# Kernel tuning notes

Measured on AMD Instinct MI355X. Metric: run time of the kernel, lower is better.

## Reference

```python
import jax, jax.numpy as jnp
import numpy as np

TAU = 10.0
EPS = 1e-6
TOP_K = 8


def setup_inputs() -> dict:
    key = jax.random.key(0)
    ks = jax.random.split(key, 5)
    D, NB, H = 1024, 512, 4096
    B, S = 4, 2048
    x = jax.random.normal(ks[0], (B, S, D), dtype=jnp.float32)
    W1 = jax.random.normal(ks[1], (H, D), dtype=jnp.float32) * (1.0 / np.sqrt(D))
    W2 = jax.random.normal(ks[2], (D, H), dtype=jnp.float32) * (1.0 / np.sqrt(H))
    ln_g = jnp.ones((D,), jnp.float32)
    ln_b = jnp.zeros((D,), jnp.float32)
    router_W = jax.random.normal(ks[3], (NB, D), dtype=jnp.float32) * 0.01
    router_b = jnp.zeros((NB,), jnp.float32)
    raw_U = jax.random.normal(ks[4], (NB, D), dtype=jnp.float32) * 0.02
    raw_V = jax.random.normal(jax.random.fold_in(key, 7), (NB, D), dtype=jnp.float32) * 0.02
    gamma = jnp.ones((1, 1, D), jnp.float32) * 0.1
    return {"x": x, "W1": W1, "W2": W2, "ln_g": ln_g, "ln_b": ln_b,
            "router_W": router_W, "router_b": router_b,
            "raw_U": raw_U, "raw_V": raw_V, "gamma": gamma}


def _layernorm(x, g, b):
    mu = jnp.mean(x, axis=-1, keepdims=True)
    var = jnp.var(x, axis=-1, keepdims=True)
    return (x - mu) * jax.lax.rsqrt(var + 1e-5) * g + b


def _unit_rows(W):
    n = jnp.linalg.norm(W, axis=1, keepdims=True)
    return W / jnp.maximum(n, EPS)


def reference(x, W1, W2, ln_g, ln_b, router_W, router_b, raw_U, raw_V, gamma):
    B, S, D = x.shape
    x_flat = x.reshape(-1, D)                      # [N, D]
    r_raw = _layernorm(x_flat, ln_g, ln_b) @ router_W.T + router_b  # [N, NB]
    r = jnp.clip(r_raw, -TAU, TAU)
    alpha = jax.nn.softplus(r)
    phi, idx = jax.lax.top_k(alpha, TOP_K)         # [N, K]
    S_sum = jnp.sum(phi, axis=-1, keepdims=True)
    Z = (phi / (S_sum + EPS)) * jnp.tanh(S_sum)    # [N, K]
    U_sel = _unit_rows(raw_U)[idx]                 # [N, K, D]
    V_sel = _unit_rows(raw_V)[idx]                 # [N, K, D]
    h_lat = jnp.einsum('nd,nkd->nk', x_flat, U_sel)
    dyn = jnp.einsum('nk,nkd->nd', h_lat * Z, V_sel).reshape(B, S, D) * gamma
    static = (jax.nn.gelu(x_flat @ W1.T, approximate=False) @ W2.T).reshape(B, S, D)
    return static + dyn
```

## Files before the change

### kernel.cpp

```cpp
#include <hip/hip_runtime.h>
#include <hip/hip_bf16.h>
#include <math.h>

#define N_TOK 8192
#define DDIM  1024
#define HDIM  4096
#define NBLK  512

typedef __bf16 bf16x8 __attribute__((ext_vector_type(8)));
typedef __bf16 bf16x4 __attribute__((ext_vector_type(4)));
typedef float  floatx4 __attribute__((ext_vector_type(4)));

__device__ __forceinline__ float wave_reduce_sum(float v) {
#pragma unroll
    for (int off = 32; off > 0; off >>= 1) v += __shfl_down(v, off, 64);
    return v;
}

__device__ __forceinline__ void gload_lds16(const void* g, void* l) {
    __builtin_amdgcn_global_load_lds((const __attribute__((address_space(1))) void*)g,
                                     (__attribute__((address_space(3))) void*)l,
                                     16, 0, 0);
}

__device__ __forceinline__ float fast_gelu(float x) {
    float ax = fabsf(x);
    float z  = ax * 0.70710678118654752f;
    float t  = __builtin_amdgcn_rcpf(fmaf(0.3275911f, z, 1.0f));
    float p  = fmaf(fmaf(fmaf(fmaf(1.061405429f, t, -1.453152027f),
                              t, 1.421413741f),
                         t, -0.284496736f),
                    t, 0.254829592f);
    p *= t;
    float e = __expf(-z * z);
    float E = fmaf(-p, e, 1.0f);
    return 0.5f * fmaf(ax, E, x);
}

__device__ __forceinline__ float fast_softplus(float r) {
    return __logf(fmaf(1.0f, __expf(r), 1.0f));
}

__device__ __forceinline__ void cast1024(const float* __restrict__ s,
                                         __bf16* __restrict__ d,
                                         size_t off, int t) {
    float4 v = ((const float4*)(s + off))[t];
    bf16x4 o;
    o.x = (__bf16)v.x; o.y = (__bf16)v.y;
    o.z = (__bf16)v.z; o.w = (__bf16)v.w;
    ((bf16x4*)(d + off))[t] = o;
}

__global__ __launch_bounds__(256) void prep_kernel(
        const float* __restrict__ x,
        const float* __restrict__ ln_g, const float* __restrict__ ln_b,
        const float* __restrict__ W1,   const float* __restrict__ W2,
        const float* __restrict__ router_W,
        const float* __restrict__ rawU, const float* __restrict__ rawV,
        __bf16* __restrict__ xb,  __bf16* __restrict__ lnb,
        __bf16* __restrict__ w1b, __bf16* __restrict__ w2b,
        __bf16* __restrict__ rwb,
        float* __restrict__ unitU, float* __restrict__ unitV) {
    int b = blockIdx.x;
    int t = threadIdx.x;

    if (b < 1024) {
        const float* src = (b < NBLK) ? rawU + (size_t)b * DDIM
                                      : rawV + (size_t)(b - NBLK) * DDIM;
        float* dst = (b < NBLK) ? unitU + (size_t)b * DDIM
                                : unitV + (size_t)(b - NBLK) * DDIM;
        float vals[4];
        float ss = 0.f;
#pragma unroll
        for (int i = 0; i < 4; i++) { vals[i] = src[t + i * 256]; ss += vals[i] * vals[i]; }
        __shared__ float red[4];
        ss = wave_reduce_sum(ss);
        if ((t & 63) == 0) red[t >> 6] = ss;
        __syncthreads();
        float tot = red[0] + red[1] + red[2] + red[3];
        float inv = 1.f / fmaxf(sqrtf(tot), 1e-6f);
#pragma unroll
        for (int i = 0; i < 4; i++) dst[t + i * 256] = vals[i] * inv;
    } else if (b < 9216) {
        int n = b - 1024;
        const float* row = x + (size_t)n * DDIM;
        float v[4];
        float s1 = 0.f, s2 = 0.f;
#pragma unroll
        for (int i = 0; i < 4; i++) {
            v[i] = row[t + i * 256];
            s1 += v[i];
            s2 += v[i] * v[i];
        }
        __shared__ float r1[4], r2[4];
        s1 = wave_reduce_sum(s1);
        s2 = wave_reduce_sum(s2);
        if ((t & 63) == 0) { r1[t >> 6] = s1; r2[t >> 6] = s2; }
        __syncthreads();
        float mu  = (r1[0] + r1[1] + r1[2] + r1[3]) * (1.f / DDIM);
        float var = (r2[0] + r2[1] + r2[2] + r2[3]) * (1.f / DDIM) - mu * mu;
        float rstd = rsqrtf(var + 1e-5f);
        __bf16* orow = lnb + (size_t)n * DDIM;
        __bf16* xrow = xb  + (size_t)n * DDIM;
#pragma unroll
        for (int i = 0; i < 4; i++) {
            int d = t + i * 256;
            orow[d] = (__bf16)((v[i] - mu) * rstd * ln_g[d] + ln_b[d]);
            xrow[d] = (__bf16)v[i];
        }
    } else if (b < 13312) {
        cast1024(W1, w1b, (size_t)(b - 9216) * 1024, t);
    } else if (b < 17408) {
        cast1024(W2, w2b, (size_t)(b - 13312) * 1024, t);
    } else {
        cast1024(router_W, rwb, (size_t)(b - 17408) * 1024, t);
    }
}

template <int MODE, int BN>
__global__ __launch_bounds__(256) void mfma_gemm(const __bf16* __restrict__ A,
                                                 const __bf16* __restrict__ B,
                                                 const float* __restrict__ bias,
                                                 void* __restrict__ Cv,
                                                 int M, int Nn, int Kk) {
    constexpr int NJ  = BN / 32;
    constexpr int NQB = BN / 64;
    __shared__ __align__(16) __bf16 As[2][128 * 32];
    __shared__ __align__(16) __bf16 Bs[2][BN * 32];

    const int t    = threadIdx.x;
    const int lane = t & 63;
    const int wave = t >> 6;
    const int wm   = wave >> 1, wn = wave & 1;
    const int lr   = lane & 15, quad = lane >> 4;
    const int m0   = blockIdx.x * 128;
    const int n0   = blockIdx.y * BN;

    const int ca0 = t & 3;
    const __bf16* Ag[2];
    const __bf16* Bg[NQB];
    int ldsOffA[2], ldsOffB[NQB];
#pragma unroll
    for (int q = 0; q < 2; q++) {
        int idx = q * 256 + t;
        Ag[q]      = A + (size_t)(m0 + (idx >> 2)) * Kk + ca0 * 8;
        ldsOffA[q] = idx * 8;
    }
#pragma unroll
    for (int q = 0; q < NQB; q++) {
        int idx = q * 256 + t;
        Bg[q]      = B + (size_t)(n0 + (idx >> 2)) * Kk + ca0 * 8;
        ldsOffB[q] = idx * 8;
    }

    int raOff[4], rbOff[NJ];
#pragma unroll
    for (int i = 0; i < 4; i++)
        raOff[i] = (wm * 64 + i * 16 + lr) * 32 + quad * 8;
#pragma unroll
    for (int j = 0; j < NJ; j++)
        rbOff[j] = (wn * (BN / 2) + j * 16 + lr) * 32 + quad * 8;

    floatx4 acc[4][NJ];
#pragma unroll
    for (int i = 0; i < 4; i++)
#pragma unroll
        for (int j = 0; j < NJ; j++) acc[i][j] = (floatx4)0.f;

#pragma unroll
    for (int q = 0; q < 2; q++)   gload_lds16(Ag[q], &As[0][ldsOffA[q]]);
#pragma unroll
    for (int q = 0; q < NQB; q++) gload_lds16(Bg[q], &Bs[0][ldsOffB[q]]);

    const int niter = Kk >> 5;
    for (int it = 0; it < niter; ++it) {
        const int cur = it & 1;
        __syncthreads();
        if (it + 1 < niter) {
            const int nk = (it + 1) << 5;
            const int nb = cur ^ 1;
#pragma unroll
            for (int q = 0; q < 2; q++)   gload_lds16(Ag[q] + nk, &As[nb][ldsOffA[q]]);
#pragma unroll
            for (int q = 0; q < NQB; q++) gload_lds16(Bg[q] + nk, &Bs[nb][ldsOffB[q]]);
        }
        bf16x8 af[4], bfr[NJ];
#pragma unroll
        for (int i = 0; i < 4; i++)  af[i]  = *(const bf16x8*)&As[cur][raOff[i]];
#pragma unroll
        for (int j = 0; j < NJ; j++) bfr[j] = *(const bf16x8*)&Bs[cur][rbOff[j]];
#pragma unroll
        for (int i = 0; i < 4; i++)
#pragma unroll
            for (int j = 0; j < NJ; j++)
                acc[i][j] = __builtin_amdgcn_mfma_f32_16x16x32_bf16(af[i], bfr[j],
                                                                    acc[i][j], 0, 0, 0);
    }

    const int mBase = m0 + wm * 64 + quad * 4;
    const int nBase = n0 + wn * (BN / 2) + lr;
#pragma unroll
    for (int i = 0; i < 4; i++) {
#pragma unroll
        for (int j = 0; j < NJ; j++) {
            int n = nBase + j * 16;
#pragma unroll
            for (int r = 0; r < 4; r++) {
                int m = mBase + i * 16 + r;
                float v = acc[i][j][r];
                if (MODE == 0) {
                    float rr = v + bias[n];
                    rr = fminf(fmaxf(rr, -10.f), 10.f);
                    ((float*)Cv)[(size_t)m * Nn + n] = fast_softplus(rr);
                } else if (MODE == 1) {
                    ((__bf16*)Cv)[(size_t)m * Nn + n] = (__bf16)fast_gelu(v);
                } else {
                    ((float*)Cv)[(size_t)m * Nn + n] += v;
                }
            }
        }
    }
}

template <int MODE, int SPLITK>
__global__ __launch_bounds__(512, 2) void mfma_gemm8v2(const __bf16* __restrict__ A,
                                                       const __bf16* __restrict__ B,
                                                       void* __restrict__ Cv,
                                                       int M, int Nn, int Kk) {
    __shared__ __align__(16) __bf16 As[2][256 * 64];
    __shared__ __align__(16) __bf16 Bs[2][256 * 64];

    const int t    = threadIdx.x;
    const int lane = t & 63;
    const int wave = t >> 6;
    const int wm   = wave >> 2;
    const int wn   = wave & 3;
    const int lr   = lane & 15, quad = lane >> 4;

    const int nbn   = Nn >> 8;
    const int nmb   = M >> 8;
    const int chunk = gridDim.x >> 3;
    const int bid   = blockIdx.x;
    const int wg    = (bid & 7) * chunk + (bid >> 3);
    const int kslc  = wg / (nmb * nbn);
    const int rem   = wg % (nmb * nbn);
    const int m0    = (rem / nbn) * 256;
    const int n0    = (rem % nbn) * 256;
    const int kseg  = Kk / SPLITK;
    const int NT    = kseg >> 6;

    const int srow = t >> 3;
    const int scb  = ((t & 7) << 4) ^ ((srow & 7) << 4);
    const __bf16* aP = A + (size_t)(m0 + srow) * Kk + (size_t)kslc * kseg + (scb >> 1);
    const __bf16* bP = B + (size_t)(n0 + srow) * Kk + (size_t)kslc * kseg + (scb >> 1);
    const int dP = srow * 64 + (t & 7) * 8;

    int aRd[2], bRd[2];
#pragma unroll
    for (int ks = 0; ks < 2; ks++) {
        int sw = ((ks * 64 + quad * 16) ^ ((lr & 7) << 4)) >> 1;
        aRd[ks] = (wm * 64 + lr) * 64 + sw;
        bRd[ks] = (wn * 32 + lr) * 64 + sw;
    }

    floatx4 acc[8][4];
#pragma unroll
    for (int i = 0; i < 8; i++)
#pragma unroll
        for (int j = 0; j < 4; j++) acc[i][j] = (floatx4)0.f;

    bf16x8 af[4][2];
    bf16x8 bfr0[2][2];
    bf16x8 bfr1[2][2];

#define STAGE_A(KT, MH, BUF)                                                        \
    _Pragma("unroll") for (int q = 0; q < 2; q++)                                   \
        gload_lds16(aP + (size_t)(KT) * 64 + (size_t)(q * 64 + (MH) * 128) * Kk,    \
                    &As[BUF][dP + (q * 64 + (MH) * 128) * 64])
#define STAGE_B(KT, NH, BUF)                                                        \
    _Pragma("unroll") for (int q = 0; q < 2; q++)                                   \
        gload_lds16(bP + (size_t)(KT) * 64 + (size_t)(q * 64 + (NH) * 128) * Kk,    \
                    &Bs[BUF][dP + (q * 64 + (NH) * 128) * 64])
#define LDA(CUR, MH)                                                                \
    _Pragma("unroll") for (int ii = 0; ii < 4; ii++)                                \
    _Pragma("unroll") for (int ks = 0; ks < 2; ks++)                                \
        af[ii][ks] = *(const bf16x8*)&As[CUR][aRd[ks] + (MH) * 8192 + ii * 1024]
#define LDB(CUR, NH, DST)                                                           \
    _Pragma("unroll") for (int jj = 0; jj < 2; jj++)                                \
    _Pragma("unroll") for (int ks = 0; ks < 2; ks++)                                \
        DST[jj][ks] = *(const bf16x8*)&Bs[CUR][bRd[ks] + ((NH) * 128 + jj * 16) * 64]
#define MM(MH, NH, BFR)                                                             \
    _Pragma("unroll") for (int ii = 0; ii < 4; ii++)                                \
    _Pragma("unroll") for (int jj = 0; jj < 2; jj++)                                \
    _Pragma("unroll") for (int ks = 0; ks < 2; ks++)                                \
        acc[(MH) * 4 + ii][(NH) * 2 + jj] =                                         \
            __builtin_amdgcn_mfma_f32_16x16x32_bf16(                                \
                af[ii][ks], BFR[jj][ks], acc[(MH) * 4 + ii][(NH) * 2 + jj], 0, 0, 0)
#define VWAIT(NSTR) asm volatile("s_waitcnt vmcnt(" NSTR ")" ::: "memory")
#define LHINT()     asm volatile("s_waitcnt lgkmcnt(8)" ::: "memory")
#define WAITL()     asm volatile("s_waitcnt lgkmcnt(0)" ::: "memory")
#define BARR()      __builtin_amdgcn_s_barrier()
#define PRIO1()     __builtin_amdgcn_s_setprio(1)
#define PRIO0()     __builtin_amdgcn_s_setprio(0)

#define TILE(KT, CUR, ST1, ST2, VM)                                                 \
    do {                                                                            \
        LDA(CUR, 0); LDB(CUR, 0, bfr0);                                             \
        if (ST1) { STAGE_A((KT) + 1, 1, ((KT) + 1) & 1); }                          \
        LHINT(); BARR(); WAITL();                                                   \
        PRIO1(); MM(0, 0, bfr0); PRIO0(); BARR();                                   \
        LDB(CUR, 1, bfr1);                                                          \
        if (ST2) { STAGE_A((KT) + 2, 0, (KT) & 1); }                                \
        BARR(); WAITL();                                                            \
        PRIO1(); MM(0, 1, bfr1); PRIO0(); BARR();                                   \
        LDA(CUR, 1);                                                                \
        if (ST2) { STAGE_B((KT) + 2, 0, (KT) & 1); }                                \
        BARR(); WAITL();                                                            \
        PRIO1(); MM(1, 1, bfr1); PRIO0(); BARR();                                   \
        if (ST2) { STAGE_B((KT) + 2, 1, (KT) & 1); }                                \
        VWAIT(VM); BARR();                                                          \
        PRIO1(); MM(1, 0, bfr0); PRIO0(); BARR();                                   \
    } while (0)

    STAGE_A(0, 0, 0); STAGE_B(0, 0, 0); STAGE_B(0, 1, 0); STAGE_A(0, 1, 0);
    STAGE_A(1, 0, 1); STAGE_B(1, 0, 1); STAGE_B(1, 1, 1);
    VWAIT("6");
    BARR();

    for (int kt = 0; kt < NT - 2; ++kt)
        TILE(kt, kt & 1, true, true, "6");
    TILE(NT - 2, (NT - 2) & 1, true, false, "0");
    TILE(NT - 1, (NT - 1) & 1, false, false, "0");

#undef STAGE_A
#undef STAGE_B
#undef LDA
#undef LDB
#undef MM
#undef VWAIT
#undef LHINT
#undef WAITL
#undef BARR
#undef PRIO1
#undef PRIO0
#undef TILE

#pragma unroll
    for (int i = 0; i < 8; i++) {
        const int mh = i >> 2, ii = i & 3;
#pragma unroll
        for (int j = 0; j < 4; j++) {
            const int nh = j >> 1, jj = j & 1;
            const int n = n0 + nh * 128 + wn * 32 + jj * 16 + lr;
#pragma unroll
            for (int r = 0; r < 4; r++) {
                const int m = m0 + mh * 128 + wm * 64 + ii * 16 + quad * 4 + r;
                const float v = acc[i][j][r];
                if (MODE == 1) {
                    ((__bf16*)Cv)[(size_t)m * Nn + n] = (__bf16)fast_gelu(v);
                } else {
                    atomicAdd(&((float*)Cv)[(size_t)m * Nn + n], v);
                }
            }
        }
    }
}

__global__ __launch_bounds__(256) void topk_dyn_kernel(
        const float* __restrict__ alpha,
        const float* __restrict__ x,
        const float* __restrict__ unitU,
        const float* __restrict__ unitV,
        const float* __restrict__ gamma,
        float* __restrict__ out) {
    int n = blockIdx.x;
    int t = threadIdx.x;
    int lane = t & 63, wid = t >> 6;

    __shared__ int   sidx[8];
    __shared__ float shz[8];
    __shared__ float red[8][4];
    __shared__ float hz[8];

    if (wid == 0) {
        const float* row = alpha + (size_t)n * NBLK;
        float v[8];
#pragma unroll
        for (int i = 0; i < 8; i++) v[i] = row[lane + i * 64];
        float topv[8];
        int   topi[8];
        for (int s = 0; s < 8; s++) {
            float bv = v[0]; int bi = 0;
#pragma unroll
            for (int i = 1; i < 8; i++)
                if (v[i] > bv) { bv = v[i]; bi = i; }
            int gidx = lane + bi * 64;
#pragma unroll
            for (int off = 1; off < 64; off <<= 1) {
                float ov = __shfl_xor(bv, off, 64);
                int   oi = __shfl_xor(gidx, off, 64);
                if (ov > bv || (ov == bv && oi < gidx)) { bv = ov; gidx = oi; }
            }
            topv[s] = bv; topi[s] = gidx;
            if ((gidx & 63) == lane) v[gidx >> 6] = -1e30f;
        }
        float S = 0.f;
#pragma unroll
        for (int s = 0; s < 8; s++) S += topv[s];
        float zscale = tanhf(S) / (S + 1e-6f);
        if (lane < 8) {
            sidx[lane] = topi[lane];
            shz[lane]  = topv[lane] * zscale;
        }
    }
    __syncthreads();

    const float* xr = x + (size_t)n * DDIM;
    float xv[4];
#pragma unroll
    for (int i = 0; i < 4; i++) xv[i] = xr[t + i * 256];

    float acc[8];
#pragma unroll
    for (int k = 0; k < 8; k++) {
        const float* ur = unitU + (size_t)sidx[k] * DDIM;
        float a = 0.f;
#pragma unroll
        for (int i = 0; i < 4; i++) a = fmaf(xv[i], ur[t + i * 256], a);
        acc[k] = a;
    }
#pragma unroll
    for (int k = 0; k < 8; k++) {
        float a = wave_reduce_sum(acc[k]);
        if (lane == 0) red[k][wid] = a;
    }
    __syncthreads();
    if (t < 8) {
        float h = red[t][0] + red[t][1] + red[t][2] + red[t][3];
        hz[t] = h * shz[t];
    }
    __syncthreads();

    float* orow = out + (size_t)n * DDIM;
#pragma unroll
    for (int i = 0; i < 4; i++) {
        int d = t + i * 256;
        float s = 0.f;
#pragma unroll
        for (int k = 0; k < 8; k++)
            s = fmaf(hz[k], unitV[(size_t)sidx[k] * DDIM + d], s);
        orow[d] = s * gamma[d];
    }
}

extern "C" void kernel_launch(void* const* d_in, const int* in_sizes, int n_in,
                              void* d_out, int out_size, void* d_ws, size_t ws_size,
                              hipStream_t stream) {
    const float* x        = (const float*)d_in[0];
    const float* W1       = (const float*)d_in[1];
    const float* W2       = (const float*)d_in[2];
    const float* ln_g     = (const float*)d_in[3];
    const float* ln_b     = (const float*)d_in[4];
    const float* router_W = (const float*)d_in[5];
    const float* router_b = (const float*)d_in[6];
    const float* raw_U    = (const float*)d_in[7];
    const float* raw_V    = (const float*)d_in[8];
    const float* gamma    = (const float*)d_in[9];
    float* out = (float*)d_out;

    char* ws = (char*)d_ws;
    __bf16* lnb   = (__bf16*)(ws);
    float*  alpha = (float*)(ws + 16777216u);
    __bf16* g1    = (__bf16*)(ws);
    __bf16* xb    = (__bf16*)(ws + 67108864u);
    __bf16* w1b   = (__bf16*)(ws + 83886080u);
    __bf16* w2b   = (__bf16*)(ws + 92274688u);
    __bf16* rwb   = (__bf16*)(ws + 100663296u);
    float*  unitU = (float*)(ws + 101711872u);
    float*  unitV = (float*)(ws + 103809024u);

    prep_kernel<<<17920, 256, 0, stream>>>(x, ln_g, ln_b, W1, W2, router_W,
                                           raw_U, raw_V, xb, lnb, w1b, w2b, rwb,
                                           unitU, unitV);

    dim3 gR(N_TOK / 128, NBLK / 64);
    mfma_gemm<0, 64><<<gR, 256, 0, stream>>>(lnb, rwb, router_b, (void*)alpha,
                                             N_TOK, NBLK, DDIM);

    topk_dyn_kernel<<<N_TOK, 256, 0, stream>>>(alpha, x, unitU, unitV, gamma, out);

    mfma_gemm8v2<1, 1><<<dim3(512), dim3(512), 0, stream>>>(xb, w1b, (void*)g1,
                                                            N_TOK, HDIM, DDIM);

    mfma_gemm8v2<2, 2><<<dim3(256), dim3(512), 0, stream>>>(g1, w2b, (void*)out,
                                                            N_TOK, DDIM, HDIM);
}
```

Before: 371.5 us.

## Add finer-grained vmcnt pipeline schedule for first GEMM and vectorize elementwise kernels

Adds a template schedule parameter to the 256x256 MFMA GEMM. The first GEMM (x·W1ᵀ with GELU) now uses a variant that waits on global-to-LDS loads at several points inside each K tile, keeping more loads in flight rather than waiting once per tile. The second GEMM keeps the old schedule. The prep and top-k/dynamic kernels are switched to float4/bf16x4 vector loads and stores to cut memory instruction count. The vmcnt thresholds are hand-tuned, so a wrong value could cause a read of LDS data that has not arrived yet.

Measured after the change: 369.2 us, median of 2. About the same (-0.6%).

```diff
diff --git a/kernel.cpp b/kernel.cpp
--- a/kernel.cpp
+++ b/kernel.cpp
@@ -69,29 +69,22 @@
                                       : rawV + (size_t)(b - NBLK) * DDIM;
         float* dst = (b < NBLK) ? unitU + (size_t)b * DDIM
                                 : unitV + (size_t)(b - NBLK) * DDIM;
-        float vals[4];
-        float ss = 0.f;
-#pragma unroll
-        for (int i = 0; i < 4; i++) { vals[i] = src[t + i * 256]; ss += vals[i] * vals[i]; }
+        float4 v = ((const float4*)src)[t];
+        float ss = v.x * v.x + v.y * v.y + v.z * v.z + v.w * v.w;
         __shared__ float red[4];
         ss = wave_reduce_sum(ss);
         if ((t & 63) == 0) red[t >> 6] = ss;
         __syncthreads();
         float tot = red[0] + red[1] + red[2] + red[3];
         float inv = 1.f / fmaxf(sqrtf(tot), 1e-6f);
-#pragma unroll
-        for (int i = 0; i < 4; i++) dst[t + i * 256] = vals[i] * inv;
+        float4 o;
+        o.x = v.x * inv; o.y = v.y * inv; o.z = v.z * inv; o.w = v.w * inv;
+        ((float4*)dst)[t] = o;
     } else if (b < 9216) {
         int n = b - 1024;
-        const float* row = x + (size_t)n * DDIM;
-        float v[4];
-        float s1 = 0.f, s2 = 0.f;
-#pragma unroll
-        for (int i = 0; i < 4; i++) {
-            v[i] = row[t + i * 256];
-            s1 += v[i];
-            s2 += v[i] * v[i];
-        }
+        float4 v = ((const float4*)(x + (size_t)n * DDIM))[t];
+        float s1 = v.x + v.y + v.z + v.w;
+        float s2 = v.x * v.x + v.y * v.y + v.z * v.z + v.w * v.w;
         __shared__ float r1[4], r2[4];
         s1 = wave_reduce_sum(s1);
         s2 = wave_reduce_sum(s2);
@@ -100,14 +93,17 @@
         float mu  = (r1[0] + r1[1] + r1[2] + r1[3]) * (1.f / DDIM);
         float var = (r2[0] + r2[1] + r2[2] + r2[3]) * (1.f / DDIM) - mu * mu;
         float rstd = rsqrtf(var + 1e-5f);
-        __bf16* orow = lnb + (size_t)n * DDIM;
-        __bf16* xrow = xb  + (size_t)n * DDIM;
-#pragma unroll
-        for (int i = 0; i < 4; i++) {
-            int d = t + i * 256;
-            orow[d] = (__bf16)((v[i] - mu) * rstd * ln_g[d] + ln_b[d]);
-            xrow[d] = (__bf16)v[i];
-        }
+        float4 g  = ((const float4*)ln_g)[t];
+        float4 bb = ((const float4*)ln_b)[t];
+        bf16x4 o, xo;
+        o.x = (__bf16)((v.x - mu) * rstd * g.x + bb.x);
+        o.y = (__bf16)((v.y - mu) * rstd * g.y + bb.y);
+        o.z = (__bf16)((v.z - mu) * rstd * g.z + bb.z);
+        o.w = (__bf16)((v.w - mu) * rstd * g.w + bb.w);
+        xo.x = (__bf16)v.x; xo.y = (__bf16)v.y;
+        xo.z = (__bf16)v.z; xo.w = (__bf16)v.w;
+        ((bf16x4*)(lnb + (size_t)n * DDIM))[t] = o;
+        ((bf16x4*)(xb  + (size_t)n * DDIM))[t] = xo;
     } else if (b < 13312) {
         cast1024(W1, w1b, (size_t)(b - 9216) * 1024, t);
     } else if (b < 17408) {
@@ -222,7 +218,7 @@
     }
 }
 
-template <int MODE, int SPLITK>
+template <int MODE, int SPLITK, int SCHED>
 __global__ __launch_bounds__(512, 2) void mfma_gemm8v2(const __bf16* __restrict__ A,
                                                        const __bf16* __restrict__ B,
                                                        void* __restrict__ Cv,
@@ -303,7 +299,26 @@
 #define PRIO1()     __builtin_amdgcn_s_setprio(1)
 #define PRIO0()     __builtin_amdgcn_s_setprio(0)
 
-#define TILE(KT, CUR, ST1, ST2, VM)                                                 \
+#define TILE3(KT, CUR, ST1, ST2, VM0, VM1, VM3)                                     \
+    do {                                                                            \
+        LDA(CUR, 0); LDB(CUR, 0, bfr0);                                             \
+        if (ST1) { STAGE_A((KT) + 1, 1, ((KT) + 1) & 1); }                          \
+        VWAIT(VM0); BARR(); WAITL();                                                \
+        PRIO1(); MM(0, 0, bfr0); PRIO0(); BARR();                                   \
+        LDB(CUR, 1, bfr1);                                                          \
+        if (ST2) { STAGE_A((KT) + 2, 0, (KT) & 1); }                                \
+        VWAIT(VM1); BARR(); WAITL();                                                \
+        PRIO1(); MM(0, 1, bfr1); PRIO0(); BARR();                                   \
+        LDA(CUR, 1);                                                                \
+        if (ST2) { STAGE_B((KT) + 2, 0, (KT) & 1); }                                \
+        BARR(); WAITL();                                                            \
+        PRIO1(); MM(1, 1, bfr1); PRIO0(); BARR();                                   \
+        if (ST2) { STAGE_B((KT) + 2, 1, (KT) & 1); }                                \
+        VWAIT(VM3); BARR();                                                         \
+        PRIO1(); MM(1, 0, bfr0); PRIO0(); BARR();                                   \
+    } while (0)
+
+#define TILE1(KT, CUR, ST1, ST2, VM)                                                \
     do {                                                                            \
         LDA(CUR, 0); LDB(CUR, 0, bfr0);                                             \
         if (ST1) { STAGE_A((KT) + 1, 1, ((KT) + 1) & 1); }                          \
@@ -324,13 +339,20 @@
 
     STAGE_A(0, 0, 0); STAGE_B(0, 0, 0); STAGE_B(0, 1, 0); STAGE_A(0, 1, 0);
     STAGE_A(1, 0, 1); STAGE_B(1, 0, 1); STAGE_B(1, 1, 1);
-    VWAIT("6");
+    if (SCHED == 0) { VWAIT("10"); } else { VWAIT("6"); }
     BARR();
 
-    for (int kt = 0; kt < NT - 2; ++kt)
-        TILE(kt, kt & 1, true, true, "6");
-    TILE(NT - 2, (NT - 2) & 1, true, false, "0");
-    TILE(NT - 1, (NT - 1) & 1, false, false, "0");
+    if (SCHED == 0) {
+        for (int kt = 0; kt < NT - 2; ++kt)
+            TILE3(kt, kt & 1, true, true, "10", "10", "10");
+        TILE3(NT - 2, (NT - 2) & 1, true, false, "10", "8", "4");
+        TILE3(NT - 1, (NT - 1) & 1, false, false, "2", "0", "0");
+    } else {
+        for (int kt = 0; kt < NT - 2; ++kt)
+            TILE1(kt, kt & 1, true, true, "6");
+        TILE1(NT - 2, (NT - 2) & 1, true, false, "0");
+        TILE1(NT - 1, (NT - 1) & 1, false, false, "0");
+    }
 
 #undef STAGE_A
 #undef STAGE_B
@@ -343,7 +365,8 @@
 #undef BARR
 #undef PRIO1
 #undef PRIO0
-#undef TILE
+#undef TILE3
+#undef TILE1
 
 #pragma unroll
     for (int i = 0; i < 8; i++) {
@@ -415,19 +438,13 @@
     }
     __syncthreads();
 
-    const float* xr = x + (size_t)n * DDIM;
-    float xv[4];
-#pragma unroll
-    for (int i = 0; i < 4; i++) xv[i] = xr[t + i * 256];
+    float4 xv = ((const float4*)(x + (size_t)n * DDIM))[t];
 
     float acc[8];
 #pragma unroll
     for (int k = 0; k < 8; k++) {
-        const float* ur = unitU + (size_t)sidx[k] * DDIM;
-        float a = 0.f;
-#pragma unroll
-        for (int i = 0; i < 4; i++) a = fmaf(xv[i], ur[t + i * 256], a);
-        acc[k] = a;
+        float4 u = ((const float4*)(unitU + (size_t)sidx[k] * DDIM))[t];
+        acc[k] = xv.x * u.x + xv.y * u.y + xv.z * u.z + xv.w * u.w;
     }
 #pragma unroll
     for (int k = 0; k < 8; k++) {
@@ -441,16 +458,20 @@
     }
     __syncthreads();
 
-    float* orow = out + (size_t)n * DDIM;
-#pragma unroll
-    for (int i = 0; i < 4; i++) {
-        int d = t + i * 256;
-        float s = 0.f;
-#pragma unroll
-        for (int k = 0; k < 8; k++)
-            s = fmaf(hz[k], unitV[(size_t)sidx[k] * DDIM + d], s);
-        orow[d] = s * gamma[d];
-    }
+    float4 s = {0.f, 0.f, 0.f, 0.f};
+#pragma unroll
+    for (int k = 0; k < 8; k++) {
+        float4 v = ((const float4*)(unitV + (size_t)sidx[k] * DDIM))[t];
+        float h = hz[k];
+        s.x = fmaf(h, v.x, s.x);
+        s.y = fmaf(h, v.y, s.y);
+        s.z = fmaf(h, v.z, s.z);
+        s.w = fmaf(h, v.w, s.w);
+    }
+    float4 g = ((const float4*)gamma)[t];
+    float4 o;
+    o.x = s.x * g.x; o.y = s.y * g.y; o.z = s.z * g.z; o.w = s.w * g.w;
+    ((float4*)(out + (size_t)n * DDIM))[t] = o;
 }
 
 extern "C" void kernel_launch(void* const* d_in, const int* in_sizes, int n_in,
@@ -489,9 +510,9 @@
 
     topk_dyn_kernel<<<N_TOK, 256, 0, stream>>>(alpha, x, unitU, unitV, gamma, out);
 
-    mfma_gemm8v2<1, 1><<<dim3(512), dim3(512), 0, stream>>>(xb, w1b, (void*)g1,
-                                                            N_TOK, HDIM, DDIM);
-
-    mfma_gemm8v2<2, 2><<<dim3(256), dim3(512), 0, stream>>>(g1, w2b, (void*)out,
-                                                            N_TOK, DDIM, HDIM);
-}
+    mfma_gemm8v2<1, 1, 0><<<dim3(512), dim3(512), 0, stream>>>(xb, w1b, (void*)g1,
+                                                               N_TOK, HDIM, DDIM);
+
+    mfma_gemm8v2<2, 2, 1><<<dim3(256), dim3(512), 0, stream>>>(g1, w2b, (void*)out,
+                                                               N_TOK, DDIM, HDIM);
+}
```
